# Performance work log

Hardware: AMD Instinct MI355X
Metric: run time of the kernel (lower is better)

The kernel has to match this reference:

```python
import jax, jax.numpy as jnp
import numpy as np
import math

ALPHA = 2.0  # surrogate-gradient sharpness from the original module

@jax.custom_vjp
def spike_fn(x):
    # Heaviside forward, atan surrogate backward (matches torch atan Function)
    return (x >= 0.0).astype(x.dtype)

def _spike_fwd(x):
    return spike_fn(x), x

def _spike_bwd(x, g):
    return (ALPHA / 2.0 / (1.0 + (ALPHA * math.pi / 2.0 * x) ** 2) * g,)

spike_fn.defvjp(_spike_fwd, _spike_bwd)

B, T, N = 32, 64, 16384

def setup_inputs() -> dict:
    key = jax.random.key(0)
    k1, k2, k3 = jax.random.split(key, 3)
    x = jax.random.normal(k1, (B, T, N), dtype=jnp.float32)
    # heterogeneous per-neuron params: thresh ~ N(0.5, 0.1), tau ~ N(2.0, 0.1)
    thresh = 0.5 + 0.1 * jax.random.normal(k2, (N,), dtype=jnp.float32)
    tau = 2.0 + 0.1 * jax.random.normal(k3, (N,), dtype=jnp.float32)
    tau_x = -jnp.log(tau - 1.0)  # nn.Parameter(-log(tau-1)) in the original
    return {"x": x, "thresh": thresh, "tau_x": tau_x}

def reference(x, thresh, tau_x):
    # x: [B, T, N]; thresh, tau_x: [N]
    sig = jax.nn.sigmoid(tau_x)          # [N], constant over timesteps
    xt = jnp.swapaxes(x, 0, 1)           # [T, B, N] for scan over T

    def step(mem, inp):
        mem = (inp - mem) * sig + mem    # leaky integration
        spike = spike_fn(mem - thresh)   # threshold fire
        mem = (1.0 - spike) * mem        # hard reset
        return mem, (spike, mem)

    mem0 = jnp.zeros_like(xt[0])         # [B, N]
    _, (spikes, mems) = jax.lax.scan(step, mem0, xt)
    # stack along dim=1 like torch.stack(..., dim=1)
    return jnp.swapaxes(spikes, 0, 1), jnp.swapaxes(mems, 0, 1)
```

## Files before the change

### kernel.cpp

```cpp
#include <hip/hip_runtime.h>
#include <math.h>


constexpr int B = 32;
constexpr int T = 64;
constexpr int N = 16384;
constexpr int N4 = N / 4;

__global__ __launch_bounds__(256) void lif_fwd_kernel(
    const float4* __restrict__ x,
    const float4* __restrict__ thresh,
    const float4* __restrict__ tau_x,
    float4* __restrict__ spikes,
    float4* __restrict__ mems)
{
    const int g = blockIdx.x * blockDim.x + threadIdx.x;
    if (g >= B * N4) return;
    const int n4 = g & (N4 - 1);
    const int b  = g >> 12;

    const float4 th = thresh[n4];
    const float4 tx = tau_x[n4];

    const double sig0 = 1.0 / (1.0 + exp(-(double)tx.x));
    const double sig1 = 1.0 / (1.0 + exp(-(double)tx.y));
    const double sig2 = 1.0 / (1.0 + exp(-(double)tx.z));
    const double sig3 = 1.0 / (1.0 + exp(-(double)tx.w));
    const double th0 = (double)th.x, th1 = (double)th.y,
                 th2 = (double)th.z, th3 = (double)th.w;

    double m0 = 0.0, m1 = 0.0, m2 = 0.0, m3 = 0.0;

    const long base = (long)b * T * N4 + n4;

#pragma unroll 4
    for (int t = 0; t < T; ++t) {
        const long idx = base + (long)t * N4;
        const float4 xv = x[idx];

        m0 = ((double)xv.x - m0) * sig0 + m0;
        m1 = ((double)xv.y - m1) * sig1 + m1;
        m2 = ((double)xv.z - m2) * sig2 + m2;
        m3 = ((double)xv.w - m3) * sig3 + m3;

        const float s0 = (m0 >= th0) ? 1.0f : 0.0f;
        const float s1 = (m1 >= th1) ? 1.0f : 0.0f;
        const float s2 = (m2 >= th2) ? 1.0f : 0.0f;
        const float s3 = (m3 >= th3) ? 1.0f : 0.0f;

        if (s0 != 0.0f) m0 = 0.0;
        if (s1 != 0.0f) m1 = 0.0;
        if (s2 != 0.0f) m2 = 0.0;
        if (s3 != 0.0f) m3 = 0.0;

        spikes[idx] = make_float4(s0, s1, s2, s3);
        mems[idx]   = make_float4((float)m0, (float)m1, (float)m2, (float)m3);
    }
}

extern "C" void kernel_launch(void* const* d_in, const int* in_sizes, int n_in,
                              void* d_out, int out_size, void* d_ws, size_t ws_size,
                              hipStream_t stream) {
    const float4* x      = (const float4*)d_in[0];
    const float4* thresh = (const float4*)d_in[1];
    const float4* tau_x  = (const float4*)d_in[2];

    float* out = (float*)d_out;
    float4* spikes = (float4*)out;
    float4* mems   = (float4*)(out + (size_t)B * T * N);

    const int total_threads = B * N4;
    const int block = 256;
    const int grid = (total_threads + block - 1) / block;

    lif_fwd_kernel<<<grid, block, 0, stream>>>(x, thresh, tau_x, spikes, mems);
}
```

Measured before the change: 366.3 us.

## Switch LIF recurrence to fp32 with nontemporal stores and deeper unroll

The per-timestep membrane recurrence and threshold compare now run in fp32 instead of double; only the one-time sigmoid is still computed in double. FMA contraction is disabled so results match the reference rounding. Outputs are written with nontemporal stores and the loop is unrolled 8 instead of 4, which lets more loads be in flight. The bounds check is dropped because the grid divides exactly. Fp32 arithmetic may differ slightly from the double path near the threshold, though it follows the reference's float semantics.

```diff
diff --git a/kernel.cpp b/kernel.cpp
--- a/kernel.cpp
+++ b/kernel.cpp
@@ -7,71 +7,76 @@
 constexpr int N = 16384;
 constexpr int N4 = N / 4;
 
+typedef float v4f __attribute__((ext_vector_type(4)));
+
 __global__ __launch_bounds__(256) void lif_fwd_kernel(
-    const float4* __restrict__ x,
-    const float4* __restrict__ thresh,
-    const float4* __restrict__ tau_x,
-    float4* __restrict__ spikes,
-    float4* __restrict__ mems)
+    const v4f* __restrict__ x,
+    const v4f* __restrict__ thresh,
+    const v4f* __restrict__ tau_x,
+    v4f* __restrict__ spikes,
+    v4f* __restrict__ mems)
 {
+#pragma clang fp contract(off)
     const int g = blockIdx.x * blockDim.x + threadIdx.x;
-    if (g >= B * N4) return;
     const int n4 = g & (N4 - 1);
     const int b  = g >> 12;
 
-    const float4 th = thresh[n4];
-    const float4 tx = tau_x[n4];
+    const v4f th = thresh[n4];
+    const v4f tx = tau_x[n4];
 
-    const double sig0 = 1.0 / (1.0 + exp(-(double)tx.x));
-    const double sig1 = 1.0 / (1.0 + exp(-(double)tx.y));
-    const double sig2 = 1.0 / (1.0 + exp(-(double)tx.z));
-    const double sig3 = 1.0 / (1.0 + exp(-(double)tx.w));
-    const double th0 = (double)th.x, th1 = (double)th.y,
-                 th2 = (double)th.z, th3 = (double)th.w;
+    const float sig0 = (float)(1.0 / (1.0 + exp(-(double)tx.x)));
+    const float sig1 = (float)(1.0 / (1.0 + exp(-(double)tx.y)));
+    const float sig2 = (float)(1.0 / (1.0 + exp(-(double)tx.z)));
+    const float sig3 = (float)(1.0 / (1.0 + exp(-(double)tx.w)));
 
-    double m0 = 0.0, m1 = 0.0, m2 = 0.0, m3 = 0.0;
+    float m0 = 0.0f, m1 = 0.0f, m2 = 0.0f, m3 = 0.0f;
 
-    const long base = (long)b * T * N4 + n4;
+    const size_t base = (size_t)b * T * N4 + n4;
+    const v4f* __restrict__ xp = x + base;
+    v4f* __restrict__ sp = spikes + base;
+    v4f* __restrict__ mp = mems + base;
 
-#pragma unroll 4
+#pragma unroll 8
     for (int t = 0; t < T; ++t) {
-        const long idx = base + (long)t * N4;
-        const float4 xv = x[idx];
+        const int off = t * N4;
+        const v4f xv = xp[off];
 
-        m0 = ((double)xv.x - m0) * sig0 + m0;
-        m1 = ((double)xv.y - m1) * sig1 + m1;
-        m2 = ((double)xv.z - m2) * sig2 + m2;
-        m3 = ((double)xv.w - m3) * sig3 + m3;
+        m0 = (xv.x - m0) * sig0 + m0;
+        m1 = (xv.y - m1) * sig1 + m1;
+        m2 = (xv.z - m2) * sig2 + m2;
+        m3 = (xv.w - m3) * sig3 + m3;
 
-        const float s0 = (m0 >= th0) ? 1.0f : 0.0f;
-        const float s1 = (m1 >= th1) ? 1.0f : 0.0f;
-        const float s2 = (m2 >= th2) ? 1.0f : 0.0f;
-        const float s3 = (m3 >= th3) ? 1.0f : 0.0f;
+        const float s0 = (m0 >= th.x) ? 1.0f : 0.0f;
+        const float s1 = (m1 >= th.y) ? 1.0f : 0.0f;
+        const float s2 = (m2 >= th.z) ? 1.0f : 0.0f;
+        const float s3 = (m3 >= th.w) ? 1.0f : 0.0f;
 
-        if (s0 != 0.0f) m0 = 0.0;
-        if (s1 != 0.0f) m1 = 0.0;
-        if (s2 != 0.0f) m2 = 0.0;
-        if (s3 != 0.0f) m3 = 0.0;
+        m0 = (s0 != 0.0f) ? 0.0f : m0;
+        m1 = (s1 != 0.0f) ? 0.0f : m1;
+        m2 = (s2 != 0.0f) ? 0.0f : m2;
+        m3 = (s3 != 0.0f) ? 0.0f : m3;
 
-        spikes[idx] = make_float4(s0, s1, s2, s3);
-        mems[idx]   = make_float4((float)m0, (float)m1, (float)m2, (float)m3);
+        v4f sv; sv.x = s0; sv.y = s1; sv.z = s2; sv.w = s3;
+        v4f mv; mv.x = m0; mv.y = m1; mv.z = m2; mv.w = m3;
+        __builtin_nontemporal_store(sv, sp + off);
+        __builtin_nontemporal_store(mv, mp + off);
     }
 }
 
 extern "C" void kernel_launch(void* const* d_in, const int* in_sizes, int n_in,
                               void* d_out, int out_size, void* d_ws, size_t ws_size,
                               hipStream_t stream) {
-    const float4* x      = (const float4*)d_in[0];
-    const float4* thresh = (const float4*)d_in[1];
-    const float4* tau_x  = (const float4*)d_in[2];
+    const v4f* x      = (const v4f*)d_in[0];
+    const v4f* thresh = (const v4f*)d_in[1];
+    const v4f* tau_x  = (const v4f*)d_in[2];
 
     float* out = (float*)d_out;
-    float4* spikes = (float4*)out;
-    float4* mems   = (float4*)(out + (size_t)B * T * N);
+    v4f* spikes = (v4f*)out;
+    v4f* mems   = (v4f*)(out + (size_t)B * T * N);
 
     const int total_threads = B * N4;
     const int block = 256;
-    const int grid = (total_threads + block - 1) / block;
+    const int grid = total_threads / block;
 
     lif_fwd_kernel<<<grid, block, 0, stream>>>(x, thresh, tau_x, spikes, mems);
 }
```

After: 383.4 us. 1.05x slower.
